# Optimization experiments

Measured on AMD Instinct MI355X. Metric: run time of the kernel, lower is better.

## Reference

```python
import jax, jax.numpy as jnp
import numpy as np

B, S, D, H, FD = 2, 2048, 1024, 16, 64
DK = D // H
ALPHA = 1.0


def _l2norm(t):
    # matches F.normalize(p=2, dim=-1): divide by max(norm, eps)
    n = jnp.linalg.norm(t, axis=-1, keepdims=True)
    return t / jnp.maximum(n, 1e-12)


def setup_inputs() -> dict:
    key = jax.random.key(0)
    ks = jax.random.split(key, 12)
    sc = 0.02
    return {
        "x": jax.random.normal(ks[0], (B, S, D), jnp.float32),
        "features": jax.random.normal(ks[1], (B, S, FD), jnp.float32),
        "requirements": jax.random.normal(ks[2], (B, S, FD), jnp.float32),
        "Wq": jax.random.normal(ks[3], (D, D), jnp.float32) * sc,
        "bq": jnp.zeros((D,), jnp.float32),
        "Wk": jax.random.normal(ks[4], (D, D), jnp.float32) * sc,
        "bk": jnp.zeros((D,), jnp.float32),
        "Wv": jax.random.normal(ks[5], (D, D), jnp.float32) * sc,
        "bv": jnp.zeros((D,), jnp.float32),
        "Wo": jax.random.normal(ks[6], (D, D), jnp.float32) * sc,
        "bo": jnp.zeros((D,), jnp.float32),
        "pos_ids": jax.random.randint(ks[7], (B, S), 0, 8),
        "causal_mask": jnp.tril(jnp.ones((S, S), bool)),
    }


def reference(x, features, requirements, Wq, bq, Wk, bk, Wv, bv, Wo, bo,
              pos_ids, causal_mask):
    # q/k/v projections -> [B, S, H, DK]
    Q = (x @ Wq + bq).reshape(B, S, H, DK)
    K = (x @ Wk + bk).reshape(B, S, H, DK)
    V = (x @ Wv + bv).reshape(B, S, H, DK)

    # scaled QK^T: [B, H, S, S]
    scores = jnp.einsum('bshd,bthd->bhst', Q, K) / np.sqrt(DK).astype(np.float32)

    # ASA bias (features_only mode): cosine compat req_i . feat_j -> [B, S, S]
    bias = jnp.einsum('bsf,btf->bst', _l2norm(requirements), _l2norm(features))
    scores = scores + ALPHA * bias[:, None, :, :]

    # causal mask (True = allowed)
    scores = jnp.where(causal_mask[None, None, :, :], scores, -jnp.inf)

    weights = jax.nn.softmax(scores, axis=-1)
    weights = jnp.nan_to_num(weights, nan=0.0)

    out = jnp.einsum('bhst,bthd->bshd', weights, V).reshape(B, S, D)
    return out @ Wo + bo
```

## Files before the change

### kernel.cpp

```cpp
#include <hip/hip_runtime.h>
#include <hip/hip_bf16.h>
#include <math.h>

#define Bb 2
#define Ss 2048
#define Dd 1024
#define Hh 16
#define DK 64
#define FD 64

#define LOG2E 1.4426950408889634f

typedef short short8 __attribute__((ext_vector_type(8)));
typedef float f32x4 __attribute__((ext_vector_type(4)));
typedef unsigned int u32;

static __device__ inline ushort f2bf(float f) {
    union { float f; unsigned u; } v; v.f = f;
    unsigned r = v.u + 0x7FFF + ((v.u >> 16) & 1);
    return (ushort)(r >> 16);
}

static __device__ inline uint cvt_pk_bf16(float lo, float hi) {
    uint r;
    asm("v_cvt_pk_bf16_f32 %0, %1, %2" : "=v"(r) : "v"(lo), "v"(hi));
    return r;
}
static __device__ inline float fexp2(float x) {
    return __builtin_amdgcn_exp2f(x);
}

static __device__ inline void gload_lds16(const ushort* g, ushort* l) {
    __builtin_amdgcn_global_load_lds((const __attribute__((address_space(1))) u32*)g,
                                     (__attribute__((address_space(3))) u32*)l, 16, 0, 0);
}

__global__ __launch_bounds__(256) void cast_bf16(const float* __restrict__ in,
                                                 ushort* __restrict__ out) {
    size_t p = (size_t)blockIdx.x * 256 + threadIdx.x;
    float2 v = *(const float2*)(in + 2 * p);
    ((uint*)out)[p] = (uint)f2bf(v.x) | ((uint)f2bf(v.y) << 16);
}

__global__ __launch_bounds__(256) void transpose_cast4(const float* __restrict__ W0,
                                                       const float* __restrict__ W1,
                                                       const float* __restrict__ W2,
                                                       const float* __restrict__ W3,
                                                       ushort* __restrict__ WT) {
    __shared__ float T[64][65];
    const float* W = blockIdx.z == 0 ? W0 : blockIdx.z == 1 ? W1 : blockIdx.z == 2 ? W2 : W3;
    ushort* dst = WT + (size_t)blockIdx.z * Dd * Dd;
    const int k0 = blockIdx.x * 64, n0 = blockIdx.y * 64;
    const int tid = threadIdx.x;
#pragma unroll
    for (int i = 0; i < 4; ++i) {
        int kr = i * 16 + (tid >> 4);
        int nc = (tid & 15) * 4;
        float4 v = *(const float4*)(W + (size_t)(k0 + kr) * Dd + n0 + nc);
        T[kr][nc] = v.x; T[kr][nc + 1] = v.y; T[kr][nc + 2] = v.z; T[kr][nc + 3] = v.w;
    }
    __syncthreads();
    int nr = tid >> 2;
    int kc = (tid & 3) * 16;
    uint pk[8];
#pragma unroll
    for (int j = 0; j < 8; ++j)
        pk[j] = (uint)f2bf(T[kc + 2 * j][nr]) | ((uint)f2bf(T[kc + 2 * j + 1][nr]) << 16);
    uint* o = (uint*)(dst + (size_t)(n0 + nr) * Dd + k0 + kc);
    *(int4*)o = *(int4*)&pk[0];
    *(int4*)(o + 4) = *(int4*)&pk[4];
}

__global__ __launch_bounds__(256) void l2norm2(const float* __restrict__ fsrc,
                                               const float* __restrict__ rsrc,
                                               float* __restrict__ fn,
                                               float* __restrict__ rn) {
    int row = blockIdx.x * 4 + (threadIdx.x >> 6);
    int lane = threadIdx.x & 63;
    const float* in = fsrc; float* out = fn; int r = row;
    if (row >= Bb * Ss) { in = rsrc; out = rn; r = row - Bb * Ss; }
    float v = in[(size_t)r * FD + lane];
    float s = v * v;
#pragma unroll
    for (int off = 32; off; off >>= 1) s += __shfl_xor(s, off, 64);
    out[(size_t)r * FD + lane] = v / fmaxf(sqrtf(s), 1e-12f);
}

__global__ __launch_bounds__(256) void pack_aux(const float* __restrict__ rn,
                                                const float* __restrict__ fn,
                                                ushort* __restrict__ Qext,
                                                ushort* __restrict__ Kext) {
    size_t p = (size_t)blockIdx.x * 256 + threadIdx.x;
    int j = (int)(p & 31);
    size_t row = p >> 5;
    int s = (int)(row & (Ss - 1));
    int bh = (int)(row >> 11);
    int b = bh >> 4;
    size_t src = ((size_t)(b * Ss + s)) * FD + j * 2;
    float2 r2 = *(const float2*)(rn + src);
    float2 f2 = *(const float2*)(fn + src);
    ((uint*)Qext)[row * 64 + 32 + j] =
        (uint)f2bf(r2.x * LOG2E) | ((uint)f2bf(r2.y * LOG2E) << 16);
    ((uint*)Kext)[row * 64 + 32 + j] = (uint)f2bf(f2.x) | ((uint)f2bf(f2.y) << 16);
}

__global__ __launch_bounds__(256) void pack_vt(const ushort* __restrict__ Vrow,
                                               ushort* __restrict__ Vt) {
    __shared__ ushort T[64][72];
    const int tid = threadIdx.x;
    const int s0 = blockIdx.x * 64;
    const int h = blockIdx.y, b = blockIdx.z;
#pragma unroll
    for (int i = 0; i < 2; ++i) {
        int f = tid + i * 256;
        int sr = f >> 3, dc = (f & 7) * 8;
        *(int4*)&T[sr][dc] =
            *(const int4*)(Vrow + ((size_t)((b * Hh + h) * Ss) + s0 + sr) * 64 + dc);
    }
    __syncthreads();
    int d = tid >> 2;
    int sg = (tid & 3) * 16;
    uint pk[8];
#pragma unroll
    for (int j = 0; j < 8; ++j)
        pk[j] = (uint)T[sg + 2 * j][d] | ((uint)T[sg + 2 * j + 1][d] << 16);
    uint* dst = (uint*)(Vt + ((size_t)((b * Hh + h) * DK + d)) * Ss + s0 + sg);
    *(int4*)dst = *(int4*)&pk[0];
    *(int4*)(dst + 4) = *(int4*)&pk[4];
}

__global__ __launch_bounds__(256) void gemm_qkv(const ushort* __restrict__ xb,
                                                const ushort* __restrict__ WT,
                                                const float* __restrict__ bq,
                                                const float* __restrict__ bk,
                                                const float* __restrict__ bv,
                                                ushort* __restrict__ Qext,
                                                ushort* __restrict__ Kext,
                                                ushort* __restrict__ Vrow) {
    __shared__ ushort smem[17408];
    ushort (*As)[64] = (ushort (*)[64])smem;
    ushort (*Bs)[64] = (ushort (*)[64])(smem + 8192);
    const int tid = threadIdx.x;
    const int lane = tid & 63, wave = tid >> 6;
    const int col = lane & 15, quad = lane >> 4;
    const int wm = wave >> 1, wn = wave & 1;
    const int id = blockIdx.x >> 3;
    const int n0 = (blockIdx.x & 7) * 128;
    const int m0 = blockIdx.y * 128;
    const ushort* BTw = WT + (size_t)id * Dd * Dd;
    const float* bias = id == 0 ? bq : id == 1 ? bk : bv;

    const int l8 = lane >> 3;
    const int srcg = (lane & 7) ^ l8;
    const ushort* aS[4]; const ushort* bS[4];
    ushort* aD[4]; ushort* bD[4];
#pragma unroll
    for (int i = 0; i < 4; ++i) {
        int r = wave * 32 + i * 8 + l8;
        aS[i] = xb  + (size_t)(m0 + r) * Dd + srcg * 8;
        bS[i] = BTw + (size_t)(n0 + r) * Dd + srcg * 8;
        aD[i] = smem + (wave * 4 + i) * 512;
        bD[i] = smem + 8192 + (wave * 4 + i) * 512;
    }
    const int xs = col & 7;

    f32x4 acc[4][4] = {};

    for (int k0 = 0; k0 < Dd; k0 += 64) {
        __syncthreads();
#pragma unroll
        for (int i = 0; i < 4; ++i) {
            gload_lds16(aS[i] + k0, aD[i]);
            gload_lds16(bS[i] + k0, bD[i]);
        }
        __syncthreads();
#pragma unroll
        for (int kk = 0; kk < 2; ++kk) {
            short8 af[4], bf[4];
#pragma unroll
            for (int i = 0; i < 4; ++i) {
                af[i] = *(const short8*)&As[wm * 64 + i * 16 + col][((kk * 4 + quad) ^ xs) * 8];
                bf[i] = *(const short8*)&Bs[wn * 64 + i * 16 + col][((kk * 4 + quad) ^ xs) * 8];
            }
#pragma unroll
            for (int i = 0; i < 4; ++i)
#pragma unroll
                for (int j = 0; j < 4; ++j)
                    acc[i][j] = __builtin_amdgcn_mfma_f32_16x16x32_bf16(af[i], bf[j], acc[i][j], 0, 0, 0);
        }
    }

    __syncthreads();
    ushort (*Ep)[136] = (ushort (*)[136])smem;
    const float scl = (id == 0) ? 0.125f * LOG2E : 1.0f;
#pragma unroll
    for (int j = 0; j < 4; ++j) {
        int n_local = wn * 64 + j * 16 + col;
        float bvl = bias[n0 + n_local];
#pragma unroll
        for (int i = 0; i < 4; ++i) {
            int mb = wm * 64 + i * 16 + quad * 4;
#pragma unroll
            for (int reg = 0; reg < 4; ++reg)
                Ep[mb + reg][n_local] = f2bf((acc[i][j][reg] + bvl) * scl);
        }
    }
    __syncthreads();
    {
        const int mrow = tid >> 1;
        const int half = tid & 1;
        const int b = m0 >> 11, s = (m0 & (Ss - 1)) + mrow;
        const int hh = (n0 >> 6) + half;
        if (id == 2) {
            ushort* drow = Vrow + ((size_t)(b * Hh + hh) * Ss + s) * 64;
#pragma unroll
            for (int k = 0; k < 8; ++k)
                *(int4*)(drow + k * 8) = *(int4*)&Ep[mrow][half * 64 + k * 8];
        } else {
            ushort* drow = (id == 0 ? Qext : Kext) + ((size_t)(b * Hh + hh) * Ss + s) * 128;
#pragma unroll
            for (int k = 0; k < 8; ++k)
                *(int4*)(drow + k * 8) = *(int4*)&Ep[mrow][half * 64 + k * 8];
        }
    }
}

__global__ __launch_bounds__(256) void gemm_out(const ushort* __restrict__ Ab,
                                                const ushort* __restrict__ BT,
                                                const float* __restrict__ bias,
                                                float* __restrict__ C) {
    __shared__ ushort As[128][64];
    __shared__ ushort Bs[128][64];
    const int tid = threadIdx.x;
    const int lane = tid & 63, wave = tid >> 6;
    const int col = lane & 15, quad = lane >> 4;
    const int wm = wave >> 1, wn = wave & 1;
    const int n0 = blockIdx.x * 128;
    const int m0 = blockIdx.y * 128;

    const int l8 = lane >> 3;
    const int srcg = (lane & 7) ^ l8;
    const ushort* aS[4]; const ushort* bS[4];
    ushort* aD[4]; ushort* bD[4];
#pragma unroll
    for (int i = 0; i < 4; ++i) {
        int r = wave * 32 + i * 8 + l8;
        aS[i] = Ab + (size_t)(m0 + r) * Dd + srcg * 8;
        bS[i] = BT + (size_t)(n0 + r) * Dd + srcg * 8;
        aD[i] = &As[0][0] + (wave * 4 + i) * 512;
        bD[i] = &Bs[0][0] + (wave * 4 + i) * 512;
    }
    const int xs = col & 7;

    f32x4 acc[4][4] = {};

    for (int k0 = 0; k0 < Dd; k0 += 64) {
        __syncthreads();
#pragma unroll
        for (int i = 0; i < 4; ++i) {
            gload_lds16(aS[i] + k0, aD[i]);
            gload_lds16(bS[i] + k0, bD[i]);
        }
        __syncthreads();
#pragma unroll
        for (int kk = 0; kk < 2; ++kk) {
            short8 af[4], bf[4];
#pragma unroll
            for (int i = 0; i < 4; ++i) {
                af[i] = *(const short8*)&As[wm * 64 + i * 16 + col][((kk * 4 + quad) ^ xs) * 8];
                bf[i] = *(const short8*)&Bs[wn * 64 + i * 16 + col][((kk * 4 + quad) ^ xs) * 8];
            }
#pragma unroll
            for (int i = 0; i < 4; ++i)
#pragma unroll
                for (int j = 0; j < 4; ++j)
                    acc[i][j] = __builtin_amdgcn_mfma_f32_16x16x32_bf16(af[i], bf[j], acc[i][j], 0, 0, 0);
        }
    }

#pragma unroll
    for (int j = 0; j < 4; ++j) {
        int n = n0 + wn * 64 + j * 16 + col;
        float bvl = bias[n];
#pragma unroll
        for (int i = 0; i < 4; ++i) {
#pragma unroll
            for (int reg = 0; reg < 4; ++reg) {
                int m = m0 + wm * 64 + i * 16 + quad * 4 + reg;
                C[(size_t)m * Dd + n] = acc[i][j][reg] + bvl;
            }
        }
    }
}

#define ABQ 128

__global__ __launch_bounds__(512) void attn_mfma13(const ushort* __restrict__ Qe,
                                                   const ushort* __restrict__ Ke,
                                                   const ushort* __restrict__ Vt,
                                                   ushort* __restrict__ Ob) {
    __shared__ ushort Ks[128][128];
    __shared__ ushort Vts[64][128];
    __shared__ ushort PsT[8][16][64];

    const int tid = threadIdx.x;
    const int wave = tid >> 6, lane = tid & 63;
    const int col = lane & 15, quad = lane >> 4;

    const int id = blockIdx.x;
    const int x = id & 7;
    const int k = id >> 3;
    const int rep = k & 1;
    const int bhi = (k >> 1) & 3;
    const int qh = k >> 3;
    const int bh = bhi * 8 + x;
    const int qt = rep ? qh : (15 - qh);
    const int b = bh >> 4, h = bh & 15;
    const int q0 = qt * ABQ;
    const int rowb = q0 + wave * 16;

    short8 qf[4];
    {
        const ushort* qp = Qe + ((size_t)bh * Ss + rowb + col) * 128 + quad * 8;
#pragma unroll
        for (int k0 = 0; k0 < 4; ++k0) qf[k0] = *(const short8*)(qp + k0 * 32);
    }

    const f32x4 zero4 = {0.f, 0.f, 0.f, 0.f};
    f32x4 oaccT[4] = {zero4, zero4, zero4, zero4};
    float lsum = 0.f;

    const ushort* Kbase = Ke + (size_t)bh * Ss * 128;
    const ushort* Vbase = Vt + (size_t)bh * 64 * Ss;
    const int xsw = col & 7;

    const ushort* kS[4]; ushort* kD[4];
#pragma unroll
    for (int i = 0; i < 4; ++i) {
        int G = i * 512 + tid;
        int r = G >> 4, g = G & 15;
        kS[i] = Kbase + (size_t)r * 128 + (g ^ (r & 7)) * 8;
        kD[i] = &Ks[0][0] + (i * 512 + wave * 64) * 8;
    }
    const ushort* vS[2]; ushort* vD[2];
#pragma unroll
    for (int i = 0; i < 2; ++i) {
        int G = i * 512 + tid;
        int r = G >> 4, g = G & 15;
        vS[i] = Vbase + (size_t)r * Ss + (g ^ (r & 7)) * 8;
        vD[i] = &Vts[0][0] + (i * 512 + wave * 64) * 8;
    }

    const int nst = qt + 1;
    for (int t2 = 0; t2 < nst; ++t2) {
        const int j0b = t2 * 128;
        const size_t ko = (size_t)j0b * 128;
        __syncthreads();
#pragma unroll
        for (int i = 0; i < 4; ++i) gload_lds16(kS[i] + ko, kD[i]);
#pragma unroll
        for (int i = 0; i < 2; ++i) gload_lds16(vS[i] + j0b, vD[i]);
        __syncthreads();

#pragma unroll
        for (int sub = 0; sub < 2; ++sub) {
            const int j0 = j0b + sub * 64;
            if (j0 > rowb + 15) continue;

            f32x4 sacc[4] = {zero4, zero4, zero4, zero4};
            __builtin_amdgcn_s_setprio(1);
#pragma unroll
            for (int c = 0; c < 4; ++c)
#pragma unroll
                for (int k0 = 0; k0 < 4; ++k0) {
                    short8 kf = *(const short8*)&Ks[sub * 64 + c * 16 + col][((k0 * 4 + quad) ^ xsw) * 8];
                    sacc[c] = __builtin_amdgcn_mfma_f32_16x16x32_bf16(kf, qf[k0], sacc[c], 0, 0, 0);
                }
            __builtin_amdgcn_s_setprio(0);

            const bool diag = (j0 + 63 >= rowb);
            if (diag) {
                const int qrow_rel = rowb + col - j0;
#pragma unroll
                for (int c = 0; c < 4; ++c)
#pragma unroll
                    for (int reg = 0; reg < 4; ++reg) {
                        float s = sacc[c][reg];
                        if (c * 16 + quad * 4 + reg > qrow_rel) s = -1e9f;
                        float p = fexp2(fminf(s, 28.853901f));
                        lsum += p;
                        sacc[c][reg] = p;
                    }
            } else {
#pragma unroll
                for (int c = 0; c < 4; ++c)
#pragma unroll
                    for (int reg = 0; reg < 4; ++reg) {
                        float p = fexp2(fminf(sacc[c][reg], 28.853901f));
                        lsum += p;
                        sacc[c][reg] = p;
                    }
            }
#pragma unroll
            for (int c = 0; c < 4; ++c) {
                uint2 pk;
                pk.x = cvt_pk_bf16(sacc[c][0], sacc[c][1]);
                pk.y = cvt_pk_bf16(sacc[c][2], sacc[c][3]);
                *(uint2*)&PsT[wave][col][((c * 2 + (quad >> 1)) ^ xsw) * 8 + (quad & 1) * 4] = pk;
            }

            __builtin_amdgcn_s_setprio(1);
#pragma unroll
            for (int k0 = 0; k0 < 2; ++k0) {
                short8 ptf = *(const short8*)&PsT[wave][col][((k0 * 4 + quad) ^ xsw) * 8];
#pragma unroll
                for (int c2 = 0; c2 < 4; ++c2) {
                    short8 vtf = *(const short8*)&Vts[c2 * 16 + col][(sub * 8 + ((k0 * 4 + quad) ^ xsw)) * 8];
                    oaccT[c2] = __builtin_amdgcn_mfma_f32_16x16x32_bf16(vtf, ptf, oaccT[c2], 0, 0, 0);
                }
            }
            __builtin_amdgcn_s_setprio(0);
        }
    }

    {
        float l = lsum;
        l += __shfl_xor(l, 16, 64);
        l += __shfl_xor(l, 32, 64);
        const float inv = 1.f / l;
        ushort* dst = Ob + ((size_t)b * Ss + rowb + col) * Dd + h * DK + quad * 4;
#pragma unroll
        for (int c2 = 0; c2 < 4; ++c2) {
            uint2 pk;
            pk.x = cvt_pk_bf16(oaccT[c2][0] * inv, oaccT[c2][1] * inv);
            pk.y = cvt_pk_bf16(oaccT[c2][2] * inv, oaccT[c2][3] * inv);
            *(uint2*)(dst + c2 * 16) = pk;
        }
    }
}

extern "C" void kernel_launch(void* const* d_in, const int* in_sizes, int n_in,
                              void* d_out, int out_size, void* d_ws, size_t ws_size,
                              hipStream_t stream) {
    const float* x            = (const float*)d_in[0];
    const float* features     = (const float*)d_in[1];
    const float* requirements = (const float*)d_in[2];
    const float* Wq = (const float*)d_in[3];
    const float* bq = (const float*)d_in[4];
    const float* Wk = (const float*)d_in[5];
    const float* bk = (const float*)d_in[6];
    const float* Wv = (const float*)d_in[7];
    const float* bv = (const float*)d_in[8];
    const float* Wo = (const float*)d_in[9];
    const float* bo = (const float*)d_in[10];

    float* out = (float*)d_out;
    float* ws = (float*)d_ws;

    ushort* xb   = (ushort*)(ws);
    ushort* WT   = (ushort*)(ws + 2097152);
    ushort* Qext = (ushort*)(ws + 4194304);
    ushort* Kext = (ushort*)(ws + 8388608);
    ushort* Vrow = (ushort*)(ws + 12582912);
    ushort* Vt   = (ushort*)(ws + 16777216);
    float*  fn   =           ws + 18874368;
    float*  rn   =           ws + 19136512;
    ushort* abb  = (ushort*)(ws + 12582912);

    cast_bf16<<<8192, 256, 0, stream>>>(x, xb);
    transpose_cast4<<<dim3(16, 16, 4), 256, 0, stream>>>(Wq, Wk, Wv, Wo, WT);
    l2norm2<<<2048, 256, 0, stream>>>(features, requirements, fn, rn);
    pack_aux<<<8192, 256, 0, stream>>>(rn, fn, Qext, Kext);

    gemm_qkv<<<dim3(24, 32), 256, 0, stream>>>(xb, WT, bq, bk, bv, Qext, Kext, Vrow);
    pack_vt<<<dim3(Ss / 64, Hh, Bb), 256, 0, stream>>>(Vrow, Vt);

    attn_mfma13<<<dim3(512), 512, 0, stream>>>(Qext, Kext, Vt, abb);

    gemm_out<<<dim3(8, 32), 256, 0, stream>>>(abb, WT + (size_t)3 * Dd * Dd, bo, out);
}
```

Measured before the change: 245.5 us.

## Fuse prep kernels, remap QKV GEMM blocks, shrink attention tiles to 64 rows

Merges the bf16 cast, weight transpose, L2 norm and aux-packing kernels into one prep launch, and computes the normalized bias features directly without intermediate fp32 buffers. The QKV GEMM block index mapping is changed so blocks on the same XCD share an n0 column slice. Attention is reworked to use 256-thread blocks with 64 query rows and 64-key tiles over 1024 blocks, aiming at better load balance and occupancy. The cost is more K/V tile reloads per query row and more synchronisation per key.

```diff
diff --git a/kernel.cpp b/kernel.cpp
--- a/kernel.cpp
+++ b/kernel.cpp
@@ -35,73 +35,75 @@
                                      (__attribute__((address_space(3))) u32*)l, 16, 0, 0);
 }
 
-__global__ __launch_bounds__(256) void cast_bf16(const float* __restrict__ in,
-                                                 ushort* __restrict__ out) {
-    size_t p = (size_t)blockIdx.x * 256 + threadIdx.x;
-    float2 v = *(const float2*)(in + 2 * p);
-    ((uint*)out)[p] = (uint)f2bf(v.x) | ((uint)f2bf(v.y) << 16);
-}
-
-__global__ __launch_bounds__(256) void transpose_cast4(const float* __restrict__ W0,
-                                                       const float* __restrict__ W1,
-                                                       const float* __restrict__ W2,
-                                                       const float* __restrict__ W3,
-                                                       ushort* __restrict__ WT) {
+__global__ __launch_bounds__(256) void prep(const float* __restrict__ x,
+                                            const float* __restrict__ features,
+                                            const float* __restrict__ requirements,
+                                            const float* __restrict__ W0,
+                                            const float* __restrict__ W1,
+                                            const float* __restrict__ W2,
+                                            const float* __restrict__ W3,
+                                            ushort* __restrict__ WT,
+                                            ushort* __restrict__ xb,
+                                            ushort* __restrict__ Qext,
+                                            ushort* __restrict__ Kext) {
     __shared__ float T[64][65];
-    const float* W = blockIdx.z == 0 ? W0 : blockIdx.z == 1 ? W1 : blockIdx.z == 2 ? W2 : W3;
-    ushort* dst = WT + (size_t)blockIdx.z * Dd * Dd;
-    const int k0 = blockIdx.x * 64, n0 = blockIdx.y * 64;
+    const int blk = blockIdx.x;
     const int tid = threadIdx.x;
-#pragma unroll
-    for (int i = 0; i < 4; ++i) {
-        int kr = i * 16 + (tid >> 4);
-        int nc = (tid & 15) * 4;
-        float4 v = *(const float4*)(W + (size_t)(k0 + kr) * Dd + n0 + nc);
-        T[kr][nc] = v.x; T[kr][nc + 1] = v.y; T[kr][nc + 2] = v.z; T[kr][nc + 3] = v.w;
-    }
-    __syncthreads();
-    int nr = tid >> 2;
-    int kc = (tid & 3) * 16;
-    uint pk[8];
-#pragma unroll
-    for (int j = 0; j < 8; ++j)
-        pk[j] = (uint)f2bf(T[kc + 2 * j][nr]) | ((uint)f2bf(T[kc + 2 * j + 1][nr]) << 16);
-    uint* o = (uint*)(dst + (size_t)(n0 + nr) * Dd + k0 + kc);
-    *(int4*)o = *(int4*)&pk[0];
-    *(int4*)(o + 4) = *(int4*)&pk[4];
-}
-
-__global__ __launch_bounds__(256) void l2norm2(const float* __restrict__ fsrc,
-                                               const float* __restrict__ rsrc,
-                                               float* __restrict__ fn,
-                                               float* __restrict__ rn) {
-    int row = blockIdx.x * 4 + (threadIdx.x >> 6);
-    int lane = threadIdx.x & 63;
-    const float* in = fsrc; float* out = fn; int r = row;
-    if (row >= Bb * Ss) { in = rsrc; out = rn; r = row - Bb * Ss; }
-    float v = in[(size_t)r * FD + lane];
-    float s = v * v;
-#pragma unroll
-    for (int off = 32; off; off >>= 1) s += __shfl_xor(s, off, 64);
-    out[(size_t)r * FD + lane] = v / fmaxf(sqrtf(s), 1e-12f);
-}
-
-__global__ __launch_bounds__(256) void pack_aux(const float* __restrict__ rn,
-                                                const float* __restrict__ fn,
-                                                ushort* __restrict__ Qext,
-                                                ushort* __restrict__ Kext) {
-    size_t p = (size_t)blockIdx.x * 256 + threadIdx.x;
-    int j = (int)(p & 31);
-    size_t row = p >> 5;
-    int s = (int)(row & (Ss - 1));
-    int bh = (int)(row >> 11);
-    int b = bh >> 4;
-    size_t src = ((size_t)(b * Ss + s)) * FD + j * 2;
-    float2 r2 = *(const float2*)(rn + src);
-    float2 f2 = *(const float2*)(fn + src);
-    ((uint*)Qext)[row * 64 + 32 + j] =
-        (uint)f2bf(r2.x * LOG2E) | ((uint)f2bf(r2.y * LOG2E) << 16);
-    ((uint*)Kext)[row * 64 + 32 + j] = (uint)f2bf(f2.x) | ((uint)f2bf(f2.y) << 16);
+
+    if (blk < 8192) {
+        size_t p = (size_t)blk * 256 + tid;
+        float2 v = *(const float2*)(x + 2 * p);
+        ((uint*)xb)[p] = (uint)f2bf(v.x) | ((uint)f2bf(v.y) << 16);
+        return;
+    }
+    if (blk < 9216) {
+        const int f = blk - 8192;
+        const int bx = f & 15, by = (f >> 4) & 15, bz = f >> 8;
+        const float* W = bz == 0 ? W0 : bz == 1 ? W1 : bz == 2 ? W2 : W3;
+        ushort* dst = WT + (size_t)bz * Dd * Dd;
+        const int k0 = bx * 64, n0 = by * 64;
+#pragma unroll
+        for (int i = 0; i < 4; ++i) {
+            int kr = i * 16 + (tid >> 4);
+            int nc = (tid & 15) * 4;
+            float4 v = *(const float4*)(W + (size_t)(k0 + kr) * Dd + n0 + nc);
+            T[kr][nc] = v.x; T[kr][nc + 1] = v.y; T[kr][nc + 2] = v.z; T[kr][nc + 3] = v.w;
+        }
+        __syncthreads();
+        int nr = tid >> 2;
+        int kc = (tid & 3) * 16;
+        uint pk[8];
+#pragma unroll
+        for (int j = 0; j < 8; ++j)
+            pk[j] = (uint)f2bf(T[kc + 2 * j][nr]) | ((uint)f2bf(T[kc + 2 * j + 1][nr]) << 16);
+        uint* o = (uint*)(dst + (size_t)(n0 + nr) * Dd + k0 + kc);
+        *(int4*)o = *(int4*)&pk[0];
+        *(int4*)(o + 4) = *(int4*)&pk[4];
+        return;
+    }
+    {
+        const int f3 = blk - 9216;
+        const int row = f3 * 4 + (tid >> 6);
+        const int lane = tid & 63;
+        const int b = row >> 11, s = row & (Ss - 1);
+        const int j = lane & 31;
+        const float* src = (lane < 32) ? features : requirements;
+        float2 v = *(const float2*)(src + (size_t)row * FD + 2 * j);
+        float ss = v.x * v.x + v.y * v.y;
+#pragma unroll
+        for (int off = 16; off; off >>= 1) ss += __shfl_xor(ss, off, 64);
+        const float inv = 1.0f / fmaxf(sqrtf(ss), 1e-12f);
+        const float scl = (lane < 32) ? inv : inv * LOG2E;
+        const uint pk = cvt_pk_bf16(v.x * scl, v.y * scl);
+        uint* dstq = (uint*)Qext;
+        uint* dstk = (uint*)Kext;
+#pragma unroll
+        for (int h = 0; h < 16; ++h) {
+            size_t rowq = ((size_t)(b * Hh + h) * Ss + s) * 64 + 32 + j;
+            if (lane < 32) dstk[rowq] = pk;
+            else           dstq[rowq] = pk;
+        }
+    }
 }
 
 __global__ __launch_bounds__(256) void pack_vt(const ushort* __restrict__ Vrow,
@@ -144,9 +146,12 @@
     const int lane = tid & 63, wave = tid >> 6;
     const int col = lane & 15, quad = lane >> 4;
     const int wm = wave >> 1, wn = wave & 1;
-    const int id = blockIdx.x >> 3;
-    const int n0 = (blockIdx.x & 7) * 128;
-    const int m0 = blockIdx.y * 128;
+    const int flat = blockIdx.x + 24 * blockIdx.y;
+    const int xcd = flat & 7;
+    const int jj = flat >> 3;
+    const int id = jj % 3;
+    const int n0 = xcd * 128;
+    const int m0 = (jj / 3) * 128;
     const ushort* BTw = WT + (size_t)id * Dd * Dd;
     const float* bias = id == 0 ? bq : id == 1 ? bk : bv;
 
@@ -293,15 +298,13 @@
     }
 }
 
-#define ABQ 128
-
-__global__ __launch_bounds__(512) void attn_mfma13(const ushort* __restrict__ Qe,
+__global__ __launch_bounds__(256) void attn_mfma15(const ushort* __restrict__ Qe,
                                                    const ushort* __restrict__ Ke,
                                                    const ushort* __restrict__ Vt,
                                                    ushort* __restrict__ Ob) {
-    __shared__ ushort Ks[128][128];
-    __shared__ ushort Vts[64][128];
-    __shared__ ushort PsT[8][16][64];
+    __shared__ ushort Ks[64][128];
+    __shared__ ushort Vts[64][64];
+    __shared__ ushort PsT[4][16][64];
 
     const int tid = threadIdx.x;
     const int wave = tid >> 6, lane = tid & 63;
@@ -309,14 +312,15 @@
 
     const int id = blockIdx.x;
     const int x = id & 7;
-    const int k = id >> 3;
-    const int rep = k & 1;
-    const int bhi = (k >> 1) & 3;
-    const int qh = k >> 3;
+    const int j = id >> 3;
+    const int half = j & 1;
+    const int bhi = ((j >> 6) & 1) * 2 + ((j >> 1) & 1);
+    const int qh = (j >> 2) & 7;
+    const int rep = (j >> 5) & 1;
     const int bh = bhi * 8 + x;
-    const int qt = rep ? qh : (15 - qh);
+    const int qt = rep ? (15 - qh) : qh;
     const int b = bh >> 4, h = bh & 15;
-    const int q0 = qt * ABQ;
+    const int q0 = qt * 128 + half * 64;
     const int rowb = q0 + wave * 16;
 
     short8 qf[4];
@@ -337,90 +341,86 @@
     const ushort* kS[4]; ushort* kD[4];
 #pragma unroll
     for (int i = 0; i < 4; ++i) {
-        int G = i * 512 + tid;
+        int G = i * 256 + tid;
         int r = G >> 4, g = G & 15;
         kS[i] = Kbase + (size_t)r * 128 + (g ^ (r & 7)) * 8;
-        kD[i] = &Ks[0][0] + (i * 512 + wave * 64) * 8;
+        kD[i] = &Ks[0][0] + (i * 256 + wave * 64) * 8;
     }
     const ushort* vS[2]; ushort* vD[2];
 #pragma unroll
     for (int i = 0; i < 2; ++i) {
-        int G = i * 512 + tid;
-        int r = G >> 4, g = G & 15;
+        int G = i * 256 + tid;
+        int r = G >> 3, g = G & 7;
         vS[i] = Vbase + (size_t)r * Ss + (g ^ (r & 7)) * 8;
-        vD[i] = &Vts[0][0] + (i * 512 + wave * 64) * 8;
-    }
-
-    const int nst = qt + 1;
-    for (int t2 = 0; t2 < nst; ++t2) {
-        const int j0b = t2 * 128;
-        const size_t ko = (size_t)j0b * 128;
+        vD[i] = &Vts[0][0] + (i * 256 + wave * 64) * 8;
+    }
+
+    const int ntiles = 2 * qt + half + 1;
+    for (int t = 0; t < ntiles; ++t) {
+        const int j0 = t * 64;
+        const size_t ko = (size_t)j0 * 128;
         __syncthreads();
 #pragma unroll
         for (int i = 0; i < 4; ++i) gload_lds16(kS[i] + ko, kD[i]);
 #pragma unroll
-        for (int i = 0; i < 2; ++i) gload_lds16(vS[i] + j0b, vD[i]);
-        __syncthreads();
-
-#pragma unroll
-        for (int sub = 0; sub < 2; ++sub) {
-            const int j0 = j0b + sub * 64;
-            if (j0 > rowb + 15) continue;
-
-            f32x4 sacc[4] = {zero4, zero4, zero4, zero4};
-            __builtin_amdgcn_s_setprio(1);
+        for (int i = 0; i < 2; ++i) gload_lds16(vS[i] + j0, vD[i]);
+        __syncthreads();
+
+        if (j0 > rowb + 15) continue;
+
+        f32x4 sacc[4] = {zero4, zero4, zero4, zero4};
+        __builtin_amdgcn_s_setprio(1);
+#pragma unroll
+        for (int c = 0; c < 4; ++c)
+#pragma unroll
+            for (int k0 = 0; k0 < 4; ++k0) {
+                short8 kf = *(const short8*)&Ks[c * 16 + col][((k0 * 4 + quad) ^ xsw) * 8];
+                sacc[c] = __builtin_amdgcn_mfma_f32_16x16x32_bf16(kf, qf[k0], sacc[c], 0, 0, 0);
+            }
+        __builtin_amdgcn_s_setprio(0);
+
+        const bool diag = (j0 + 63 >= rowb);
+        if (diag) {
+            const int qrow_rel = rowb + col - j0;
 #pragma unroll
             for (int c = 0; c < 4; ++c)
 #pragma unroll
-                for (int k0 = 0; k0 < 4; ++k0) {
-                    short8 kf = *(const short8*)&Ks[sub * 64 + c * 16 + col][((k0 * 4 + quad) ^ xsw) * 8];
-                    sacc[c] = __builtin_amdgcn_mfma_f32_16x16x32_bf16(kf, qf[k0], sacc[c], 0, 0, 0);
+                for (int reg = 0; reg < 4; ++reg) {
+                    float s = sacc[c][reg];
+                    if (c * 16 + quad * 4 + reg > qrow_rel) s = -1e9f;
+                    float p = fexp2(fminf(s, 28.853901f));
+                    lsum += p;
+                    sacc[c][reg] = p;
                 }
-            __builtin_amdgcn_s_setprio(0);
-
-            const bool diag = (j0 + 63 >= rowb);
-            if (diag) {
-                const int qrow_rel = rowb + col - j0;
-#pragma unroll
-                for (int c = 0; c < 4; ++c)
-#pragma unroll
-                    for (int reg = 0; reg < 4; ++reg) {
-                        float s = sacc[c][reg];
-                        if (c * 16 + quad * 4 + reg > qrow_rel) s = -1e9f;
-                        float p = fexp2(fminf(s, 28.853901f));
-                        lsum += p;
-                        sacc[c][reg] = p;
-                    }
-            } else {
-#pragma unroll
-                for (int c = 0; c < 4; ++c)
-#pragma unroll
-                    for (int reg = 0; reg < 4; ++reg) {
-                        float p = fexp2(fminf(sacc[c][reg], 28.853901f));
-                        lsum += p;
-                        sacc[c][reg] = p;
-                    }
+        } else {
+#pragma unroll
+            for (int c = 0; c < 4; ++c)
+#pragma unroll
+                for (int reg = 0; reg < 4; ++reg) {
+                    float p = fexp2(fminf(sacc[c][reg], 28.853901f));
+                    lsum += p;
+                    sacc[c][reg] = p;
+                }
+        }
+#pragma unroll
+        for (int c = 0; c < 4; ++c) {
+            uint2 pk;
+            pk.x = cvt_pk_bf16(sacc[c][0], sacc[c][1]);
+            pk.y = cvt_pk_bf16(sacc[c][2], sacc[c][3]);
+            *(uint2*)&PsT[wave][col][((c * 2 + (quad >> 1)) ^ xsw) * 8 + (quad & 1) * 4] = pk;
+        }
+
+        __builtin_amdgcn_s_setprio(1);
+#pragma unroll
+        for (int k0 = 0; k0 < 2; ++k0) {
+            short8 ptf = *(const short8*)&PsT[wave][col][((k0 * 4 + quad) ^ xsw) * 8];
+#pragma unroll
+            for (int c2 = 0; c2 < 4; ++c2) {
+                short8 vtf = *(const short8*)&Vts[c2 * 16 + col][((k0 * 4 + quad) ^ xsw) * 8];
+                oaccT[c2] = __builtin_amdgcn_mfma_f32_16x16x32_bf16(vtf, ptf, oaccT[c2], 0, 0, 0);
             }
-#pragma unroll
-            for (int c = 0; c < 4; ++c) {
-                uint2 pk;
-                pk.x = cvt_pk_bf16(sacc[c][0], sacc[c][1]);
-                pk.y = cvt_pk_bf16(sacc[c][2], sacc[c][3]);
-                *(uint2*)&PsT[wave][col][((c * 2 + (quad >> 1)) ^ xsw) * 8 + (quad & 1) * 4] = pk;
-            }
-
-            __builtin_amdgcn_s_setprio(1);
-#pragma unroll
-            for (int k0 = 0; k0 < 2; ++k0) {
-                short8 ptf = *(const short8*)&PsT[wave][col][((k0 * 4 + quad) ^ xsw) * 8];
-#pragma unroll
-                for (int c2 = 0; c2 < 4; ++c2) {
-                    short8 vtf = *(const short8*)&Vts[c2 * 16 + col][(sub * 8 + ((k0 * 4 + quad) ^ xsw)) * 8];
-                    oaccT[c2] = __builtin_amdgcn_mfma_f32_16x16x32_bf16(vtf, ptf, oaccT[c2], 0, 0, 0);
-                }
-            }
-            __builtin_amdgcn_s_setprio(0);
-        }
+        }
+        __builtin_amdgcn_s_setprio(0);
     }
 
     {
@@ -463,19 +463,15 @@
     ushort* Kext = (ushort*)(ws + 8388608);
     ushort* Vrow = (ushort*)(ws + 12582912);
     ushort* Vt   = (ushort*)(ws + 16777216);
-    float*  fn   =           ws + 18874368;
-    float*  rn   =           ws + 19136512;
     ushort* abb  = (ushort*)(ws + 12582912);
 
-    cast_bf16<<<8192, 256, 0, stream>>>(x, xb);
-    transpose_cast4<<<dim3(16, 16, 4), 256, 0, stream>>>(Wq, Wk, Wv, Wo, WT);
-    l2norm2<<<2048, 256, 0, stream>>>(features, requirements, fn, rn);
-    pack_aux<<<8192, 256, 0, stream>>>(rn, fn, Qext, Kext);
+    prep<<<10240, 256, 0, stream>>>(x, features, requirements, Wq, Wk, Wv, Wo,
+                                    WT, xb, Qext, Kext);
 
     gemm_qkv<<<dim3(24, 32), 256, 0, stream>>>(xb, WT, bq, bk, bv, Qext, Kext, Vrow);
     pack_vt<<<dim3(Ss / 64, Hh, Bb), 256, 0, stream>>>(Vrow, Vt);
 
-    attn_mfma13<<<dim3(512), 512, 0, stream>>>(Qext, Kext, Vt, abb);
+    attn_mfma15<<<dim3(1024), 256, 0, stream>>>(Qext, Kext, Vt, abb);
 
     gemm_out<<<dim3(8, 32), 256, 0, stream>>>(abb, WT + (size_t)3 * Dd * Dd, bo, out);
 }
```

Measured after the change: 240.1 us. -2.2%, faster.
